# Kernel tuning notes

Measured on AMD Instinct MI355X. Metric: run time of the kernel, lower is better.

Reference implementation:

```python
import jax, jax.numpy as jnp
import numpy as np

B, TX, TZ, DX, DZ, DATT, DMID, H, DOUT = 8, 1024, 1024, 1024, 1024, 64, 64, 16, 1024


def setup_inputs() -> dict:
    key = jax.random.key(0)
    ks = jax.random.split(key, 10)
    s = 0.02
    return {
        "x": jax.random.normal(ks[0], (B, TX, DX), jnp.float32),
        "z": jax.random.normal(ks[1], (B, TZ, DZ), jnp.float32),
        "Wq": jax.random.normal(ks[2], (H, DX, DATT), jnp.float32) * s,
        "bq": jax.random.normal(ks[3], (H, DATT), jnp.float32) * s,
        "Wk": jax.random.normal(ks[4], (H, DZ, DATT), jnp.float32) * s,
        "bk": jax.random.normal(ks[5], (H, DATT), jnp.float32) * s,
        "Wv": jax.random.normal(ks[6], (H, DZ, DMID), jnp.float32) * s,
        "bv": jax.random.normal(ks[7], (H, DMID), jnp.float32) * s,
        "Wp": jax.random.normal(ks[8], (H * DMID, DOUT), jnp.float32) * s,
        "bp": jax.random.normal(ks[9], (DOUT,), jnp.float32) * s,
        "mask": jnp.tril(jnp.ones((TX, TZ), dtype=bool)),  # causal
    }


def reference(x, z, Wq, bq, Wk, bk, Wv, bv, Wp, bp, mask):
    # Per-head projections (heads batched via stacked weights). bhxe = batch, head, x-pos, feat
    Q = jnp.einsum('bxd,hde->bhxe', x, Wq) + bq[None, :, None, :]
    K = jnp.einsum('bzd,hde->bhze', z, Wk) + bk[None, :, None, :]
    V = jnp.einsum('bzd,hde->bhze', z, Wv) + bv[None, :, None, :]
    # Scores, mask (set ~mask to -inf), then scale by 1/sqrt(Datt) (as original: mask before scale)
    S = jnp.einsum('bhxe,bhze->bhxz', Q, K)
    S = jnp.where(mask[None, None, :, :], S, -jnp.inf) * (1.0 / jnp.sqrt(jnp.asarray(DATT, S.dtype)))
    A = jax.nn.softmax(S, axis=-1)
    y = jnp.einsum('bhxz,bhze->bhxe', A, V)          # [B, H, Tx, Dmid]
    y_concat = y.transpose(0, 2, 1, 3).reshape(B, TX, H * DMID)  # concat heads
    return y_concat @ Wp + bp
```

## Files before the change

### kernel.cpp

```cpp
#include <hip/hip_runtime.h>
#include <stdint.h>


typedef float    f32x4  __attribute__((ext_vector_type(4)));
typedef __bf16   bf16x8 __attribute__((ext_vector_type(8)));
typedef unsigned short u16x4 __attribute__((ext_vector_type(4)));
typedef unsigned short u16x8 __attribute__((ext_vector_type(8)));

#define MASKNEG (-3.0e38f)
#define QSCALE_F (0.125f * 1.4426950408889634f)

__device__ __forceinline__ unsigned short f2bf(float f) {
  unsigned int u = __float_as_uint(f);
  u += 0x7fffu + ((u >> 16) & 1u);
  return (unsigned short)(u >> 16);
}

__device__ __forceinline__ void gload16(const void* g, void* s) {
  const __attribute__((address_space(1))) unsigned int* gp =
      (const __attribute__((address_space(1))) unsigned int*)(uintptr_t)g;
  __attribute__((address_space(3))) unsigned int* lp =
      (__attribute__((address_space(3))) unsigned int*)(unsigned int)(uintptr_t)s;
  __builtin_amdgcn_global_load_lds(gp, lp, 16, 0, 0);
}

__device__ __forceinline__ f32x4 mfma16(bf16x8 a, bf16x8 b, f32x4 c) {
  return __builtin_amdgcn_mfma_f32_16x16x32_bf16(a, b, c, 0, 0, 0);
}


__global__ __launch_bounds__(256) void k_cvt2(const float* __restrict__ x,
                                              const float* __restrict__ z,
                                              unsigned short* __restrict__ out) {
  int i = blockIdx.x * 256 + threadIdx.x;
  const int stride = gridDim.x * 256;
  for (; i < 2097152; i += stride) {
    const float* in = (i < 1048576) ? (x + (size_t)i * 8) : (z + (size_t)(i - 1048576) * 8);
    const f32x4* p = (const f32x4*)in;
    f32x4 a = p[0], b = p[1];
    u16x8 o;
    o[0] = f2bf(a[0]); o[1] = f2bf(a[1]); o[2] = f2bf(a[2]); o[3] = f2bf(a[3]);
    o[4] = f2bf(b[0]); o[5] = f2bf(b[1]); o[6] = f2bf(b[2]); o[7] = f2bf(b[3]);
    *(u16x8*)(out + (size_t)i * 8) = o;
  }
}

__global__ __launch_bounds__(256) void k_pack(const float* __restrict__ Wq,
                                              const float* __restrict__ Wk,
                                              const float* __restrict__ Wv,
                                              const float* __restrict__ Wp,
                                              unsigned short* __restrict__ Oq,
                                              unsigned short* __restrict__ Ok,
                                              unsigned short* __restrict__ Ov,
                                              unsigned short* __restrict__ Op) {
  __shared__ float tile[64][65];
  const int t = threadIdx.x;
  const int zid = blockIdx.z;
  if (zid < 3) {
    const float* W = zid == 0 ? Wq : (zid == 1 ? Wk : Wv);
    unsigned short* O = zid == 0 ? Oq : (zid == 1 ? Ok : Ov);
    const int h = blockIdx.x, d0 = blockIdx.y * 64;
    const int ee = t & 63, r0 = t >> 6;
#pragma unroll
    for (int dd = r0; dd < 64; dd += 4)
      tile[dd][ee] = W[(h * 1024 + d0 + dd) * 64 + ee];
    __syncthreads();
    const int d = t & 63, e0 = t >> 6;
#pragma unroll
    for (int e = e0; e < 64; e += 4)
      O[(h * 64 + e) * 1024 + d0 + d] = f2bf(tile[d][e]);
  } else {
    const int k0 = blockIdx.x * 64, n0 = blockIdx.y * 64;
    const int nn = t & 63, r0 = t >> 6;
#pragma unroll
    for (int kk = r0; kk < 64; kk += 4)
      tile[kk][nn] = Wp[(k0 + kk) * 1024 + n0 + nn];
    __syncthreads();
    const int kk = t & 63, e0 = t >> 6;
#pragma unroll
    for (int n2 = e0; n2 < 64; n2 += 4)
      Op[(n0 + n2) * 1024 + k0 + kk] = f2bf(tile[kk][n2]);
  }
}

__device__ __forceinline__ void gemm_body(const unsigned short* __restrict__ A,
                                          const unsigned short* __restrict__ Bt,
                                          const float* __restrict__ bias,
                                          void* __restrict__ outp,
                                          int mode, float oscale,
                                          int brow, int bcol,
                                          unsigned short* As, unsigned short* Bs) {
  const int tid = threadIdx.x;
  const int l = tid & 63, w = tid >> 6;
  const int lrow = l & 15, lk = l >> 4;
  const int wr = (w >> 1) * 128, wc = (w & 1) * 64;

  const int arow = tid >> 2;
  const int asrc = ((tid & 3) ^ ((arow >> 1) & 3)) * 8;
  const unsigned short* ag0 = A + (size_t)(brow + arow) * 1024 + asrc;
  const unsigned short* bg0 = Bt + (size_t)(bcol + arow) * 1024 + asrc;

  int aoff[8], boff[4];
#pragma unroll
  for (int m = 0; m < 8; m++) {
    int row = wr + m * 16 + lrow;
    aoff[m] = row * 64 + ((lk ^ ((row >> 1) & 3)) << 4);
  }
#pragma unroll
  for (int n = 0; n < 4; n++) {
    int col = wc + n * 16 + lrow;
    boff[n] = col * 64 + ((lk ^ ((col >> 1) & 3)) << 4);
  }

  f32x4 acc[8][4];
#pragma unroll
  for (int n = 0; n < 4; n++) {
    float bv = bias[bcol + wc + n * 16 + lrow];
#pragma unroll
    for (int m = 0; m < 8; m++) acc[m][n] = (f32x4){bv, bv, bv, bv};
  }

#define STAGE_G(kt, slot)                                                  \
  {                                                                        \
    char* asb = (char*)As + (slot) * 16384 + w * 1024;                     \
    char* bsb = (char*)Bs + (slot) * 8192 + w * 1024;                      \
    gload16(ag0 + (kt) * 32,          asb);                                \
    gload16(ag0 + (kt) * 32 + 65536,  asb + 4096);                         \
    gload16(ag0 + (kt) * 32 + 131072, asb + 8192);                         \
    gload16(ag0 + (kt) * 32 + 196608, asb + 12288);                        \
    gload16(bg0 + (kt) * 32,          bsb);                                \
    gload16(bg0 + (kt) * 32 + 65536,  bsb + 4096);                         \
  }

  STAGE_G(0, 0)
  STAGE_G(1, 1)
  asm volatile("s_waitcnt vmcnt(6)" ::: "memory");
  __builtin_amdgcn_s_barrier();
  __builtin_amdgcn_sched_barrier(0);

  int s0 = 0, s2 = 2;
#pragma unroll 1
  for (int kt = 0; kt < 32; kt++) {
    if (kt < 30) STAGE_G(kt + 2, s2)
    const char* ab = (const char*)As + s0 * 16384;
    const char* bb = (const char*)Bs + s0 * 8192;
    bf16x8 bfr[4];
#pragma unroll
    for (int n = 0; n < 4; n++) bfr[n] = *(const bf16x8*)(bb + boff[n]);
#pragma unroll
    for (int m = 0; m < 8; m++) {
      bf16x8 af = *(const bf16x8*)(ab + aoff[m]);
#pragma unroll
      for (int n = 0; n < 4; n++)
        acc[m][n] = mfma16(af, bfr[n], acc[m][n]);
    }
    if (kt < 31) {
      if (kt < 30) {
        asm volatile("s_waitcnt vmcnt(6)" ::: "memory");
      } else {
        asm volatile("s_waitcnt vmcnt(0)" ::: "memory");
      }
      __builtin_amdgcn_s_barrier();
      __builtin_amdgcn_sched_barrier(0);
    }
    s0 = (s0 == 2) ? 0 : s0 + 1;
    s2 = (s2 == 2) ? 0 : s2 + 1;
  }
#undef STAGE_G

  if (mode == 0) {
    unsigned short* C = (unsigned short*)outp;
#pragma unroll
    for (int m = 0; m < 8; m++) {
      int r = brow + wr + m * 16 + 4 * lk;
#pragma unroll
      for (int n = 0; n < 4; n++) {
        int c = bcol + wc + n * 16 + lrow;
        unsigned short* p = C + ((r >> 10) * 16 + (c >> 6)) * 65536 + (r & 1023) * 64 + (c & 63);
#pragma unroll
        for (int j = 0; j < 4; j++) p[j * 64] = f2bf(acc[m][n][j] * oscale);
      }
    }
  } else if (mode == 2) {
    unsigned short* C = (unsigned short*)outp;
#pragma unroll
    for (int m = 0; m < 8; m++) {
      int r = brow + wr + m * 16 + 4 * lk;
#pragma unroll
      for (int n = 0; n < 4; n++) {
        int c = bcol + wc + n * 16 + lrow;
        u16x4 o;
#pragma unroll
        for (int j = 0; j < 4; j++) o[j] = f2bf(acc[m][n][j]);
        *(u16x4*)(C + ((r >> 10) * 16 + (c >> 6)) * 65536 + (c & 63) * 1024 + (r & 1023)) = o;
      }
    }
  } else {
    float* C = (float*)outp;
#pragma unroll
    for (int m = 0; m < 8; m++) {
      int r = brow + wr + m * 16 + 4 * lk;
#pragma unroll
      for (int n = 0; n < 4; n++) {
        int c = bcol + wc + n * 16 + lrow;
#pragma unroll
        for (int j = 0; j < 4; j++) C[(r + j) * 1024 + c] = acc[m][n][j];
      }
    }
  }
}

__global__ __launch_bounds__(256, 2) void k_gemm_qkv(const unsigned short* __restrict__ Xb,
                                                     const unsigned short* __restrict__ Zb,
                                                     const unsigned short* __restrict__ Wqkv,
                                                     const float* __restrict__ bq,
                                                     const float* __restrict__ bk,
                                                     const float* __restrict__ bv,
                                                     unsigned short* __restrict__ Qp,
                                                     unsigned short* __restrict__ Kp,
                                                     unsigned short* __restrict__ Vtp) {
  __shared__ unsigned short As[24576];
  __shared__ unsigned short Bs[12288];
  const int brow = blockIdx.x * 256;
  const int cg = blockIdx.y;
  const int seg = cg >> 3;
  const int bcol = (cg & 7) * 128;
  const unsigned short* A = (seg == 0) ? Xb : Zb;
  const unsigned short* Bt = Wqkv + (size_t)seg * 1048576;
  const float* bias = (seg == 0) ? bq : (seg == 1 ? bk : bv);
  void* outp = (seg == 0) ? (void*)Qp : (seg == 1 ? (void*)Kp : (void*)Vtp);
  const int mode = (seg == 2) ? 2 : 0;
  const float oscale = (seg == 0) ? QSCALE_F : 1.0f;
  gemm_body(A, Bt, bias, outp, mode, oscale, brow, bcol, As, Bs);
}

__global__ __launch_bounds__(256, 2) void k_gemm(const unsigned short* __restrict__ A,
                                                 const unsigned short* __restrict__ Bt,
                                                 const float* __restrict__ bias,
                                                 void* __restrict__ outp,
                                                 int mode, float oscale) {
  __shared__ unsigned short As[24576];
  __shared__ unsigned short Bs[12288];
  gemm_body(A, Bt, bias, outp, mode, oscale, blockIdx.x * 256, blockIdx.y * 128, As, Bs);
}

__global__ __launch_bounds__(256, 2) void k_attn(const unsigned short* __restrict__ Qh,
                                                 const unsigned short* __restrict__ Kh,
                                                 const unsigned short* __restrict__ Vth,
                                                 unsigned short* __restrict__ Y) {
  __shared__ unsigned short Ks[16384];
  __shared__ unsigned short Vs[16384];
  __shared__ unsigned short Ps[8192];

  const int tid = threadIdx.x, l = tid & 63, w = tid >> 6;
  const int lrow = l & 15, lk = l >> 4;
  const int bh = blockIdx.x;
  const int pp = blockIdx.y;

  const unsigned short* Qb = Qh + bh * 65536;
  const unsigned short* Kb = Kh + bh * 65536;
  const unsigned short* Vb = Vth + bh * 65536;

  bf16x8 ones;
#pragma unroll
  for (int j = 0; j < 8; j++) ones[j] = (__bf16)1.0f;

  const int krl = l >> 3;
  const int kgp = l & 7;
  const unsigned short* kgsrc = Kb + (w * 32 + krl) * 64 + ((kgp ^ krl) * 8);
  const int vrl = l >> 4;
  const int vgp = l & 15;
  const int vr0 = w * 16 + 0 * 4 + vrl;
  const int vr1 = w * 16 + 1 * 4 + vrl;
  const int vr2 = w * 16 + 2 * 4 + vrl;
  const int vr3 = w * 16 + 3 * 4 + vrl;
  const int voff0 = vr0 * 1024 + ((vgp ^ (vr0 & 15)) * 8);
  const int voff1 = vr1 * 1024 + ((vgp ^ (vr1 & 15)) * 8);
  const int voff2 = vr2 * 1024 + ((vgp ^ (vr2 & 15)) * 8);
  const int voff3 = vr3 * 1024 + ((vgp ^ (vr3 & 15)) * 8);

  char* pw = (char*)Ps + w * 4096;

  const int b = bh >> 4, h = bh & 15;

#pragma unroll 1
  for (int hp = 0; hp < 2; hp++) {
    const int qi = hp == 0 ? (7 - pp) : pp;
    const int qw = qi * 128 + w * 32;
    const int qmax = qw + 31;

    bf16x8 qf[2][2];
#pragma unroll
    for (int qn = 0; qn < 2; qn++) {
      const unsigned short* qp = Qb + (qw + qn * 16 + lrow) * 64 + lk * 8;
      qf[qn][0] = *(const bf16x8*)qp;
      qf[qn][1] = *(const bf16x8*)(qp + 32);
    }

    float mm[2];
    f32x4 lsum[2], yacc[2][4];
#pragma unroll
    for (int qn = 0; qn < 2; qn++) {
      mm[qn] = MASKNEG;
      lsum[qn] = (f32x4){0.f, 0.f, 0.f, 0.f};
#pragma unroll
      for (int ef = 0; ef < 4; ef++) yacc[qn][ef] = (f32x4){0.f, 0.f, 0.f, 0.f};
    }

    const int nt = qi + 1;

    {
      char* kb = (char*)Ks + w * 4096;
      char* vb2 = (char*)Vs + w * 4096;
      gload16(kgsrc + 0,    kb);
      gload16(kgsrc + 512,  kb + 1024);
      gload16(kgsrc + 1024, kb + 2048);
      gload16(kgsrc + 1536, kb + 3072);
      gload16(Vb + voff0, vb2);
      gload16(Vb + voff1, vb2 + 1024);
      gload16(Vb + voff2, vb2 + 2048);
      gload16(Vb + voff3, vb2 + 3072);
    }
    __syncthreads();

#pragma unroll 1
    for (int t = 0; t < nt; t++) {
      const int z0 = t * 128;
      const int cur = t & 1;
      if (t < nt - 1) {
        const int zn = (t + 1) * 128;
        char* kb = (char*)Ks + (cur ^ 1) * 16384 + w * 4096;
        char* vb2 = (char*)Vs + (cur ^ 1) * 16384 + w * 4096;
        const unsigned short* kgt = kgsrc + zn * 64;
        gload16(kgt + 0,    kb);
        gload16(kgt + 512,  kb + 1024);
        gload16(kgt + 1024, kb + 2048);
        gload16(kgt + 1536, kb + 3072);
        gload16(Vb + voff0 + zn, vb2);
        gload16(Vb + voff1 + zn, vb2 + 1024);
        gload16(Vb + voff2 + zn, vb2 + 2048);
        gload16(Vb + voff3 + zn, vb2 + 3072);
      }

      if (z0 <= qmax) {
        const char* kbase = (const char*)Ks + cur * 16384;
        const char* vbase = (const char*)Vs + cur * 16384;

        f32x4 s[2][8];
#pragma unroll
        for (int qn = 0; qn < 2; qn++)
#pragma unroll
          for (int zf = 0; zf < 8; zf++) s[qn][zf] = (f32x4){0.f, 0.f, 0.f, 0.f};
#pragma unroll
        for (int zf = 0; zf < 8; zf++) {
          int zr = zf * 16 + lrow;
#pragma unroll
          for (int kf = 0; kf < 2; kf++) {
            bf16x8 kfr = *(const bf16x8*)(kbase + zr * 128 + (((kf * 4 + lk) ^ (zr & 7)) << 4));
            s[0][zf] = mfma16(kfr, qf[0][kf], s[0][zf]);
            s[1][zf] = mfma16(kfr, qf[1][kf], s[1][zf]);
          }
        }

        if (z0 + 127 > qw) {
#pragma unroll
          for (int qn = 0; qn < 2; qn++) {
            int qg = qw + qn * 16 + lrow;
#pragma unroll
            for (int zf = 0; zf < 8; zf++) {
              int zb = z0 + zf * 16 + 4 * lk;
#pragma unroll
              for (int j = 0; j < 4; j++)
                if (zb + j > qg) s[qn][zf][j] = MASKNEG;
            }
          }
        }

#pragma unroll
        for (int qn = 0; qn < 2; qn++) {
          f32x4 r4 = s[qn][0];
#pragma unroll
          for (int zf = 1; zf < 8; zf++)
#pragma unroll
            for (int j = 0; j < 4; j++) r4[j] = fmaxf(r4[j], s[qn][zf][j]);
          float rm = fmaxf(fmaxf(r4[0], r4[1]), fmaxf(r4[2], r4[3]));
          rm = fmaxf(rm, __shfl_xor(rm, 16));
          rm = fmaxf(rm, __shfl_xor(rm, 32));

          if (__any(rm > mm[qn] + 8.f)) {
            float mn = fmaxf(mm[qn], rm);
            float a = __builtin_amdgcn_exp2f(mm[qn] - mn);
            mm[qn] = mn;
            f32x4 av;
#pragma unroll
            for (int j = 0; j < 4; j++)
              av[j] = __shfl(a, (l & 48) | (lk * 4 + j));
            lsum[qn] *= av;
#pragma unroll
            for (int ef = 0; ef < 4; ef++) yacc[qn][ef] *= av;
          }
          float mk = mm[qn];
#pragma unroll
          for (int zf = 0; zf < 8; zf++)
#pragma unroll
            for (int j = 0; j < 4; j++)
              s[qn][zf][j] = __builtin_amdgcn_exp2f(s[qn][zf][j] - mk);
        }

#pragma unroll
        for (int hf = 0; hf < 2; hf++) {
          if (z0 + hf * 64 <= qmax) {
#pragma unroll
            for (int qn = 0; qn < 2; qn++) {
              int q = qn * 16 + lrow;
              char* rowp = pw + q * 128;
#pragma unroll
              for (int zf2 = 0; zf2 < 4; zf2++) {
                int zfg = hf * 4 + zf2;
                u16x4 o;
#pragma unroll
                for (int j = 0; j < 4; j++) o[j] = f2bf(s[qn][zfg][j]);
                int g = zf2 * 2 + (lk >> 1);
                *(u16x4*)(rowp + ((g ^ (q & 7)) << 4) + (lk & 1) * 8) = o;
              }
            }

            asm volatile("s_waitcnt lgkmcnt(0)" ::: "memory");
            __builtin_amdgcn_sched_barrier(0);

            bf16x8 pf[2][2];
#pragma unroll
            for (int qn = 0; qn < 2; qn++)
#pragma unroll
              for (int kf = 0; kf < 2; kf++)
                pf[qn][kf] = *(const bf16x8*)(pw + (qn * 16 + lrow) * 128 + (((kf * 4 + lk) ^ (lrow & 7)) << 4));

#pragma unroll
            for (int qn = 0; qn < 2; qn++)
#pragma unroll
              for (int kf = 0; kf < 2; kf++)
                lsum[qn] = mfma16(pf[qn][kf], ones, lsum[qn]);

#pragma unroll
            for (int ef = 0; ef < 4; ef++) {
              int er = ef * 16 + lrow;
#pragma unroll
              for (int kf = 0; kf < 2; kf++) {
                int g = hf * 8 + kf * 4 + lk;
                bf16x8 vf = *(const bf16x8*)(vbase + er * 256 + ((g ^ (er & 15)) << 4));
                yacc[0][ef] = mfma16(pf[0][kf], vf, yacc[0][ef]);
                yacc[1][ef] = mfma16(pf[1][kf], vf, yacc[1][ef]);
              }
            }
          }
        }
      }

      __syncthreads();
    }

#pragma unroll
    for (int qn = 0; qn < 2; qn++) {
      f32x4 rinv;
#pragma unroll
      for (int j = 0; j < 4; j++) rinv[j] = 1.0f / lsum[qn][j];
#pragma unroll
      for (int ef = 0; ef < 4; ef++) {
        int col = h * 64 + ef * 16 + lrow;
#pragma unroll
        for (int j = 0; j < 4; j++) {
          int x = qw + qn * 16 + lk * 4 + j;
          Y[(b * 1024 + x) * 1024 + col] = f2bf(yacc[qn][ef][j] * rinv[j]);
        }
      }
    }
  }
}

extern "C" void kernel_launch(void* const* d_in, const int* in_sizes, int n_in,
                              void* d_out, int out_size, void* d_ws, size_t ws_size,
                              hipStream_t stream) {
  const float* x  = (const float*)d_in[0];
  const float* z  = (const float*)d_in[1];
  const float* Wq = (const float*)d_in[2];
  const float* bq = (const float*)d_in[3];
  const float* Wk = (const float*)d_in[4];
  const float* bk = (const float*)d_in[5];
  const float* Wv = (const float*)d_in[6];
  const float* bv = (const float*)d_in[7];
  const float* Wp = (const float*)d_in[8];
  const float* bp = (const float*)d_in[9];
  (void)in_sizes; (void)n_in; (void)out_size; (void)ws_size;

  char* ws = (char*)d_ws;
  unsigned short* Xb  = (unsigned short*)(ws + 0);
  unsigned short* Zb  = (unsigned short*)(ws + 16777216);
  unsigned short* Wqt = (unsigned short*)(ws + 33554432);
  unsigned short* Wkt = (unsigned short*)(ws + 35651584);
  unsigned short* Wvt = (unsigned short*)(ws + 37748736);
  unsigned short* Wpt = (unsigned short*)(ws + 39845888);
  unsigned short* Qp  = (unsigned short*)(ws + 41943040);
  unsigned short* Kp  = (unsigned short*)(ws + 58720256);
  unsigned short* Vtp = (unsigned short*)(ws + 75497472);

  k_cvt2<<<dim3(2048), dim3(256), 0, stream>>>(x, z, Xb);
  k_pack<<<dim3(16, 16, 4), dim3(256), 0, stream>>>(Wq, Wk, Wv, Wp, Wqt, Wkt, Wvt, Wpt);

  k_gemm_qkv<<<dim3(32, 24), dim3(256), 0, stream>>>(Xb, Zb, Wqt, bq, bk, bv, Qp, Kp, Vtp);

  k_attn<<<dim3(128, 4), dim3(256), 0, stream>>>(Qp, Kp, Vtp, Xb );

  k_gemm<<<dim3(32, 8), dim3(256), 0, stream>>>(Xb, Wpt, bp, d_out, 3, 1.0f);
}
```

Before: 149.8 us.

## Replace QKV projection GEMM with 256x256-tile, 8-wave double-buffered kernel

Adds a new QKV projection kernel that uses 512 threads (8 waves) per block and a 256x256 output tile with K-step 64. The shared-memory tiles are double-buffered, loads go straight to LDS with an XOR swizzle, and each k-step is split into four quarter-phases. Global loads are interleaved with MFMA work, and s_setprio raises priority around the MFMA sections. The larger tile halves the number of blocks and increases operand reuse per block, aiming to cut global/LDS traffic and overlap loads better. The cost is one block per CU (more LDS, launch_bounds 512,1) and fewer waves in the tail.

```diff
diff --git a/kernel.cpp b/kernel.cpp
--- a/kernel.cpp
+++ b/kernel.cpp
@@ -83,6 +83,172 @@
   }
 }
 
+__global__ __launch_bounds__(512, 1) void k_gemm_qkv8(const unsigned short* __restrict__ Xb,
+                                                      const unsigned short* __restrict__ Zb,
+                                                      const unsigned short* __restrict__ Wqkv,
+                                                      const float* __restrict__ bq,
+                                                      const float* __restrict__ bk,
+                                                      const float* __restrict__ bv,
+                                                      unsigned short* __restrict__ Qp,
+                                                      unsigned short* __restrict__ Kp,
+                                                      unsigned short* __restrict__ Vtp) {
+  __shared__ unsigned short As[32768];
+  __shared__ unsigned short Bs[32768];
+
+  const int tid = threadIdx.x;
+  const int l = tid & 63, w = tid >> 6;
+  const int lrow = l & 15, lk = l >> 4;
+  const int wr2 = w >> 2, wc2 = w & 3;
+
+  const int brow = blockIdx.x * 256;
+  const int cg = blockIdx.y;
+  const int seg = cg >> 2;
+  const int bcol = (cg & 3) * 256;
+  const unsigned short* A = (seg == 0) ? Xb : Zb;
+  const unsigned short* Bt = Wqkv + (size_t)seg * 1048576;
+  const float* bias = (seg == 0) ? bq : (seg == 1 ? bk : bv);
+  const int mode = (seg == 2) ? 2 : 0;
+  const float oscale = (seg == 0) ? QSCALE_F : 1.0f;
+
+  const int srow = tid >> 3;
+  const int presw = ((tid & 7) ^ (srow & 7)) * 8;
+  const unsigned short* agp = A + (size_t)(brow + srow) * 1024 + presw;
+  const unsigned short* bgp = Bt + (size_t)(bcol + srow) * 1024 + presw;
+
+  const int axor = lrow & 7;
+  const int albase = wr2 * 16384 + lrow * 128;
+  const int blbase = (wc2 >> 1) * 16384 + ((wc2 & 1) * 64 + lrow) * 128;
+
+  f32x4 acc[8][4];
+#pragma unroll
+  for (int n = 0; n < 4; n++) {
+    float bv = bias[bcol + wc2 * 64 + n * 16 + lrow];
+#pragma unroll
+    for (int m = 0; m < 8; m++) acc[m][n] = (f32x4){bv, bv, bv, bv};
+  }
+
+#define STG_A(half, ktn, dbn)                                                      \
+  {                                                                                \
+    char* d = (char*)As + (dbn) * 32768 + (half) * 16384 + w * 1024;               \
+    gload16(agp + (size_t)((half) * 128) * 1024 + (ktn) * 64, d);                  \
+    gload16(agp + (size_t)((half) * 128 + 64) * 1024 + (ktn) * 64, d + 8192);      \
+  }
+#define STG_B(half, ktn, dbn)                                                      \
+  {                                                                                \
+    char* d = (char*)Bs + (dbn) * 32768 + (half) * 16384 + w * 1024;               \
+    gload16(bgp + (size_t)((half) * 128) * 1024 + (ktn) * 64, d);                  \
+    gload16(bgp + (size_t)((half) * 128 + 64) * 1024 + (ktn) * 64, d + 8192);      \
+  }
+
+  STG_A(0, 0, 0) STG_A(1, 0, 0) STG_B(0, 0, 0) STG_B(1, 0, 0)
+  asm volatile("s_waitcnt vmcnt(0)" ::: "memory");
+  __builtin_amdgcn_s_barrier();
+  __builtin_amdgcn_sched_barrier(0);
+
+#pragma unroll 1
+  for (int kt = 0; kt < 16; kt++) {
+    const int db = kt & 1;
+    const char* AB = (const char*)As + db * 32768;
+    const char* BB = (const char*)Bs + db * 32768;
+    bf16x8 afr[4], bfr[4];
+
+#pragma unroll
+    for (int n = 0; n < 4; n++)
+      bfr[n] = *(const bf16x8*)(BB + blbase + n * 2048 + ((lk ^ axor) << 4));
+#pragma unroll
+    for (int m = 0; m < 4; m++)
+      afr[m] = *(const bf16x8*)(AB + albase + m * 2048 + ((lk ^ axor) << 4));
+    if (kt < 15) { STG_A(0, kt + 1, db ^ 1) STG_A(1, kt + 1, db ^ 1) }
+    __builtin_amdgcn_s_setprio(1);
+#pragma unroll
+    for (int m = 0; m < 4; m++)
+#pragma unroll
+      for (int n = 0; n < 4; n++)
+        acc[m][n] = mfma16(afr[m], bfr[n], acc[m][n]);
+    __builtin_amdgcn_s_setprio(0);
+    __builtin_amdgcn_s_barrier();
+    __builtin_amdgcn_sched_barrier(0);
+
+#pragma unroll
+    for (int m = 0; m < 4; m++)
+      afr[m] = *(const bf16x8*)(AB + albase + 8192 + m * 2048 + ((lk ^ axor) << 4));
+    if (kt < 15) { STG_B(0, kt + 1, db ^ 1) STG_B(1, kt + 1, db ^ 1) }
+    __builtin_amdgcn_s_setprio(1);
+#pragma unroll
+    for (int m = 0; m < 4; m++)
+#pragma unroll
+      for (int n = 0; n < 4; n++)
+        acc[4 + m][n] = mfma16(afr[m], bfr[n], acc[4 + m][n]);
+    __builtin_amdgcn_s_setprio(0);
+    __builtin_amdgcn_s_barrier();
+    __builtin_amdgcn_sched_barrier(0);
+
+#pragma unroll
+    for (int n = 0; n < 4; n++)
+      bfr[n] = *(const bf16x8*)(BB + blbase + n * 2048 + (((4 + lk) ^ axor) << 4));
+#pragma unroll
+    for (int m = 0; m < 4; m++)
+      afr[m] = *(const bf16x8*)(AB + albase + 8192 + m * 2048 + (((4 + lk) ^ axor) << 4));
+    __builtin_amdgcn_s_setprio(1);
+#pragma unroll
+    for (int m = 0; m < 4; m++)
+#pragma unroll
+      for (int n = 0; n < 4; n++)
+        acc[4 + m][n] = mfma16(afr[m], bfr[n], acc[4 + m][n]);
+    __builtin_amdgcn_s_setprio(0);
+    __builtin_amdgcn_s_barrier();
+    __builtin_amdgcn_sched_barrier(0);
+
+#pragma unroll
+    for (int m = 0; m < 4; m++)
+      afr[m] = *(const bf16x8*)(AB + albase + m * 2048 + (((4 + lk) ^ axor) << 4));
+    __builtin_amdgcn_s_setprio(1);
+#pragma unroll
+    for (int m = 0; m < 4; m++)
+#pragma unroll
+      for (int n = 0; n < 4; n++)
+        acc[m][n] = mfma16(afr[m], bfr[n], acc[m][n]);
+    __builtin_amdgcn_s_setprio(0);
+
+    if (kt < 15) {
+      asm volatile("s_waitcnt vmcnt(0)" ::: "memory");
+    }
+    __builtin_amdgcn_s_barrier();
+    __builtin_amdgcn_sched_barrier(0);
+  }
+#undef STG_A
+#undef STG_B
+
+  if (mode == 0) {
+    unsigned short* C = (seg == 0) ? Qp : Kp;
+#pragma unroll
+    for (int m = 0; m < 8; m++) {
+      int r = brow + wr2 * 128 + m * 16 + 4 * lk;
+#pragma unroll
+      for (int n = 0; n < 4; n++) {
+        int c = bcol + wc2 * 64 + n * 16 + lrow;
+        unsigned short* p = C + ((r >> 10) * 16 + (c >> 6)) * 65536 + (r & 1023) * 64 + (c & 63);
+#pragma unroll
+        for (int j = 0; j < 4; j++) p[j * 64] = f2bf(acc[m][n][j] * oscale);
+      }
+    }
+  } else {
+    unsigned short* C = Vtp;
+#pragma unroll
+    for (int m = 0; m < 8; m++) {
+      int r = brow + wr2 * 128 + m * 16 + 4 * lk;
+#pragma unroll
+      for (int n = 0; n < 4; n++) {
+        int c = bcol + wc2 * 64 + n * 16 + lrow;
+        u16x4 o;
+#pragma unroll
+        for (int j = 0; j < 4; j++) o[j] = f2bf(acc[m][n][j]);
+        *(u16x4*)(C + ((r >> 10) * 16 + (c >> 6)) * 65536 + (c & 63) * 1024 + (r & 1023)) = o;
+      }
+    }
+  }
+}
+
 __device__ __forceinline__ void gemm_body(const unsigned short* __restrict__ A,
                                           const unsigned short* __restrict__ Bt,
                                           const float* __restrict__ bias,
@@ -168,70 +334,19 @@
   }
 #undef STAGE_G
 
-  if (mode == 0) {
-    unsigned short* C = (unsigned short*)outp;
+  if (mode == 3) {
+    float* C = (float*)outp;
 #pragma unroll
     for (int m = 0; m < 8; m++) {
       int r = brow + wr + m * 16 + 4 * lk;
 #pragma unroll
       for (int n = 0; n < 4; n++) {
         int c = bcol + wc + n * 16 + lrow;
-        unsigned short* p = C + ((r >> 10) * 16 + (c >> 6)) * 65536 + (r & 1023) * 64 + (c & 63);
-#pragma unroll
-        for (int j = 0; j < 4; j++) p[j * 64] = f2bf(acc[m][n][j] * oscale);
-      }
-    }
-  } else if (mode == 2) {
-    unsigned short* C = (unsigned short*)outp;
-#pragma unroll
-    for (int m = 0; m < 8; m++) {
-      int r = brow + wr + m * 16 + 4 * lk;
-#pragma unroll
-      for (int n = 0; n < 4; n++) {
-        int c = bcol + wc + n * 16 + lrow;
-        u16x4 o;
-#pragma unroll
-        for (int j = 0; j < 4; j++) o[j] = f2bf(acc[m][n][j]);
-        *(u16x4*)(C + ((r >> 10) * 16 + (c >> 6)) * 65536 + (c & 63) * 1024 + (r & 1023)) = o;
-      }
-    }
-  } else {
-    float* C = (float*)outp;
-#pragma unroll
-    for (int m = 0; m < 8; m++) {
-      int r = brow + wr + m * 16 + 4 * lk;
-#pragma unroll
-      for (int n = 0; n < 4; n++) {
-        int c = bcol + wc + n * 16 + lrow;
 #pragma unroll
         for (int j = 0; j < 4; j++) C[(r + j) * 1024 + c] = acc[m][n][j];
       }
     }
   }
-}
-
-__global__ __launch_bounds__(256, 2) void k_gemm_qkv(const unsigned short* __restrict__ Xb,
-                                                     const unsigned short* __restrict__ Zb,
-                                                     const unsigned short* __restrict__ Wqkv,
-                                                     const float* __restrict__ bq,
-                                                     const float* __restrict__ bk,
-                                                     const float* __restrict__ bv,
-                                                     unsigned short* __restrict__ Qp,
-                                                     unsigned short* __restrict__ Kp,
-                                                     unsigned short* __restrict__ Vtp) {
-  __shared__ unsigned short As[24576];
-  __shared__ unsigned short Bs[12288];
-  const int brow = blockIdx.x * 256;
-  const int cg = blockIdx.y;
-  const int seg = cg >> 3;
-  const int bcol = (cg & 7) * 128;
-  const unsigned short* A = (seg == 0) ? Xb : Zb;
-  const unsigned short* Bt = Wqkv + (size_t)seg * 1048576;
-  const float* bias = (seg == 0) ? bq : (seg == 1 ? bk : bv);
-  void* outp = (seg == 0) ? (void*)Qp : (seg == 1 ? (void*)Kp : (void*)Vtp);
-  const int mode = (seg == 2) ? 2 : 0;
-  const float oscale = (seg == 0) ? QSCALE_F : 1.0f;
-  gemm_body(A, Bt, bias, outp, mode, oscale, brow, bcol, As, Bs);
 }
 
 __global__ __launch_bounds__(256, 2) void k_gemm(const unsigned short* __restrict__ A,
@@ -506,7 +621,7 @@
   k_cvt2<<<dim3(2048), dim3(256), 0, stream>>>(x, z, Xb);
   k_pack<<<dim3(16, 16, 4), dim3(256), 0, stream>>>(Wq, Wk, Wv, Wp, Wqt, Wkt, Wvt, Wpt);
 
-  k_gemm_qkv<<<dim3(32, 24), dim3(256), 0, stream>>>(Xb, Zb, Wqt, bq, bk, bv, Qp, Kp, Vtp);
+  k_gemm_qkv8<<<dim3(32, 12), dim3(512), 0, stream>>>(Xb, Zb, Wqt, bq, bk, bv, Qp, Kp, Vtp);
 
   k_attn<<<dim3(128, 4), dim3(256), 0, stream>>>(Qp, Kp, Vtp, Xb );
 
```

Result: slower. 153.1 us (+2.2%).
